# Kernel tuning notes

Measured on AMD Instinct MI355X. Metric: run time of the kernel, lower is better.

Reference implementation:

```python
import jax, jax.numpy as jnp
import numpy as np

N = 100000
D = 100
E = 1600000


def setup_inputs() -> dict:
    key = jax.random.key(0)
    k1, k2, k3, k4 = jax.random.split(key, 4)
    embedding = jax.random.normal(k1, (N, D), dtype=jnp.float32)
    adj_rows = jax.random.randint(k2, (E,), 0, N, dtype=jnp.int32)
    adj_cols = jax.random.randint(k3, (E,), 0, N, dtype=jnp.int32)
    adj_vals = jax.random.uniform(k4, (E,), dtype=jnp.float32)
    return {
        "embedding": embedding,
        "adj_rows": adj_rows,
        "adj_cols": adj_cols,
        "adj_vals": adj_vals,
        "layer_num": 3,
    }


def _spmm(rows, cols, vals, x):
    # sparse [N,N] @ dense [N,D] via gather + weighted segment-sum scatter
    msgs = x[cols] * vals[:, None]           # [E, D]
    return jax.ops.segment_sum(msgs, rows, num_segments=N)  # [N, D]


def reference(embedding, adj_rows, adj_cols, adj_vals, layer_num):
    # out = sum_{i=0}^{layer_num} A^i x  (accumulate hops, including layer 0)
    h = embedding
    acc = embedding
    for _ in range(layer_num):
        h = _spmm(adj_rows, adj_cols, adj_vals, h)
        acc = acc + h
    return acc
```

## Files before the change

kernel.cpp:

```cpp
#include <hip/hip_runtime.h>


#define NODES 100000
#define DIM 100
#define DIM4 25
#define CH 16
#define BSHIFT 8
#define NBUCKETS ((NODES + 255) >> 8)
#define NPAD (NBUCKETS << BSHIFT)

typedef _Float16 half4_t __attribute__((ext_vector_type(4)));
typedef _Float16 half8_t __attribute__((ext_vector_type(8)));

__global__ void cvt_hist_kernel(const float4* __restrict__ emb, half4_t* __restrict__ x0,
                                const int* __restrict__ rows, int* __restrict__ bktCount, int E) {
    __shared__ int h[NBUCKETS];
    for (int i = threadIdx.x; i < NBUCKETS; i += blockDim.x) h[i] = 0;
    __syncthreads();
    int stride = gridDim.x * blockDim.x;
    int gid = blockIdx.x * blockDim.x + threadIdx.x;
    for (int i = gid; i < NODES * 32; i += stride) {
        int r = i >> 5, c = i & 31;
        half4_t hv;
        if (c < 25) {
            float4 f = emb[r * 25 + c];
            hv.x = (_Float16)f.x; hv.y = (_Float16)f.y;
            hv.z = (_Float16)f.z; hv.w = (_Float16)f.w;
        } else {
            hv.x = (_Float16)0.f; hv.y = (_Float16)0.f;
            hv.z = (_Float16)0.f; hv.w = (_Float16)0.f;
        }
        x0[i] = hv;
    }
    for (int e = gid; e < E; e += stride)
        atomicAdd(&h[rows[e] >> BSHIFT], 1);
    __syncthreads();
    for (int i = threadIdx.x; i < NBUCKETS; i += blockDim.x)
        if (h[i]) atomicAdd(&bktCount[i], h[i]);
}

__global__ void pass1_kernel(const int* __restrict__ rows, const int* __restrict__ cols,
                             const float* __restrict__ vals,
                             const int* __restrict__ bktCount, int* __restrict__ gCur,
                             int* __restrict__ bktStart,
                             int2* __restrict__ staging, int E) {
    __shared__ int cnt[NBUCKETS];
    __shared__ int bst[NBUCKETS];
    __shared__ int sc[512];
    int t = threadIdx.x;
    for (int i = t; i < NBUCKETS; i += 512) cnt[i] = 0;
    __syncthreads();
    int chunk = (E + gridDim.x - 1) / gridDim.x;
    int s = blockIdx.x * chunk;
    int e = min(E, s + chunk);
    for (int i = s + t; i < e; i += 512)
        atomicAdd(&cnt[rows[i] >> BSHIFT], 1);
    int v = (t < NBUCKETS) ? bktCount[t] : 0;
    sc[t] = v;
    __syncthreads();
    for (int off = 1; off < 512; off <<= 1) {
        int x = (t >= off) ? sc[t - off] : 0;
        __syncthreads();
        sc[t] += x;
        __syncthreads();
    }
    int excl = sc[t] - v;
    if (blockIdx.x == 0) {
        if (t < NBUCKETS) bktStart[t] = excl;
        if (t == 0) bktStart[NBUCKETS] = E;
    }
    if (t < NBUCKETS) {
        int c = cnt[t];
        bst[t] = excl + (c ? atomicAdd(&gCur[t], c) : 0);
        cnt[t] = 0;
    }
    __syncthreads();
    for (int i = s + t; i < e; i += 512) {
        int r = rows[i];
        int b = r >> BSHIFT;
        int pos = bst[b] + atomicAdd(&cnt[b], 1);
        staging[pos] = make_int2(cols[i] | ((r & 255) << 17), __float_as_int(vals[i]));
    }
}

__global__ void pass2_kernel(const int* __restrict__ bktStart, const int2* __restrict__ staging,
                             int* __restrict__ rowstart, int2* __restrict__ csr) {
    __shared__ int hist[256];
    __shared__ int cur[256];
    int b = blockIdx.x, t = threadIdx.x;
    int s = bktStart[b], e = bktStart[b + 1];
    if (t < 256) hist[t] = 0;
    __syncthreads();
    for (int i = s + t; i < e; i += 512)
        atomicAdd(&hist[(staging[i].x >> 17) & 255], 1);
    __syncthreads();
    int v = (t < 256) ? hist[t] : 0;
    if (t < 256) cur[t] = v;
    __syncthreads();
    for (int off = 1; off < 256; off <<= 1) {
        int x = (t >= off && t < 256) ? cur[t - off] : 0;
        __syncthreads();
        if (t < 256) cur[t] += x;
        __syncthreads();
    }
    if (t < 256) {
        int excl = cur[t] - v;
        rowstart[(b << BSHIFT) + t] = s + excl;
        hist[t] = excl;
    }
    __syncthreads();
    for (int i = s + t; i < e; i += 512) {
        int2 rec = staging[i];
        int lr = (rec.x >> 17) & 255;
        int p = atomicAdd(&hist[lr], 1);
        csr[s + p] = make_int2(rec.x & 0x1FFFF, rec.y);
    }
}

__global__ void gather_mid4_kernel(const int* __restrict__ rowstart,
                                   const int2* __restrict__ csr,
                                   const half8_t* __restrict__ x,
                                   half8_t* __restrict__ h) {
    int gid = blockIdx.x * blockDim.x + threadIdx.x;
    int row = gid >> 4, lane = gid & 15;
    if (row >= NODES) return;
    int s = rowstart[row], e = rowstart[row + 1];
    float acc[8] = {0.f, 0.f, 0.f, 0.f, 0.f, 0.f, 0.f, 0.f};
    int i = s;
    for (; i + 3 < e; i += 4) {
        int2 r0 = csr[i], r1 = csr[i + 1], r2 = csr[i + 2], r3 = csr[i + 3];
        half8_t a0 = x[((size_t)r0.x << 4) + lane];
        half8_t a1 = x[((size_t)r1.x << 4) + lane];
        half8_t a2 = x[((size_t)r2.x << 4) + lane];
        half8_t a3 = x[((size_t)r3.x << 4) + lane];
        float v0 = __int_as_float(r0.y), v1 = __int_as_float(r1.y);
        float v2 = __int_as_float(r2.y), v3 = __int_as_float(r3.y);
        #pragma unroll
        for (int k = 0; k < 8; ++k)
            acc[k] += v0 * (float)a0[k] + v1 * (float)a1[k]
                    + v2 * (float)a2[k] + v3 * (float)a3[k];
    }
    for (; i < e; ++i) {
        int2 r0 = csr[i];
        half8_t a0 = x[((size_t)r0.x << 4) + lane];
        float v0 = __int_as_float(r0.y);
        #pragma unroll
        for (int k = 0; k < 8; ++k) acc[k] += v0 * (float)a0[k];
    }
    half8_t hv;
    #pragma unroll
    for (int k = 0; k < 8; ++k) hv[k] = (_Float16)acc[k];
    h[((size_t)row << 4) + lane] = hv;
}

__global__ void gather_mid8_kernel(const int* __restrict__ rowstart,
                                   const int2* __restrict__ csr,
                                   const half8_t* __restrict__ x,
                                   half8_t* __restrict__ h) {
    int gid = blockIdx.x * blockDim.x + threadIdx.x;
    int row = gid >> 4, lane = gid & 15;
    if (row >= NODES) return;
    int s = rowstart[row], e = rowstart[row + 1];
    float acc[8] = {0.f, 0.f, 0.f, 0.f, 0.f, 0.f, 0.f, 0.f};
    int i = s;
    for (; i + 7 < e; i += 8) {
        int2 rr[8];
        #pragma unroll
        for (int j = 0; j < 8; ++j) rr[j] = csr[i + j];
        half8_t aa[8];
        #pragma unroll
        for (int j = 0; j < 8; ++j) aa[j] = x[((size_t)rr[j].x << 4) + lane];
        #pragma unroll
        for (int j = 0; j < 8; ++j) {
            float v = __int_as_float(rr[j].y);
            #pragma unroll
            for (int k = 0; k < 8; ++k) acc[k] += v * (float)aa[j][k];
        }
    }
    for (; i < e; ++i) {
        int2 r0 = csr[i];
        half8_t a0 = x[((size_t)r0.x << 4) + lane];
        float v0 = __int_as_float(r0.y);
        #pragma unroll
        for (int k = 0; k < 8; ++k) acc[k] += v0 * (float)a0[k];
    }
    half8_t hv;
    #pragma unroll
    for (int k = 0; k < 8; ++k) hv[k] = (_Float16)acc[k];
    h[((size_t)row << 4) + lane] = hv;
}

__global__ void gather_last_kernel(const int* __restrict__ rowstart,
                                   const int2* __restrict__ csr,
                                   const half8_t* __restrict__ x,
                                   const half8_t* __restrict__ x0,
                                   const half8_t* __restrict__ h1,
                                   const half8_t* __restrict__ h2,
                                   float4* __restrict__ out) {
    int gid = blockIdx.x * blockDim.x + threadIdx.x;
    int row = gid >> 4, lane = gid & 15;
    if (row >= NODES) return;
    int s = rowstart[row], e = rowstart[row + 1];
    float acc[8] = {0.f, 0.f, 0.f, 0.f, 0.f, 0.f, 0.f, 0.f};
    int i = s;
    for (; i + 7 < e; i += 8) {
        int2 rr[8];
        #pragma unroll
        for (int j = 0; j < 8; ++j) rr[j] = csr[i + j];
        half8_t aa[8];
        #pragma unroll
        for (int j = 0; j < 8; ++j) aa[j] = x[((size_t)rr[j].x << 4) + lane];
        #pragma unroll
        for (int j = 0; j < 8; ++j) {
            float v = __int_as_float(rr[j].y);
            #pragma unroll
            for (int k = 0; k < 8; ++k) acc[k] += v * (float)aa[j][k];
        }
    }
    for (; i < e; ++i) {
        int2 r0 = csr[i];
        half8_t a0 = x[((size_t)r0.x << 4) + lane];
        float v0 = __int_as_float(r0.y);
        #pragma unroll
        for (int k = 0; k < 8; ++k) acc[k] += v0 * (float)a0[k];
    }
    size_t pidx = ((size_t)row << 4) + lane;
    half8_t xe = x0[pidx], a1 = h1[pidx], a2 = h2[pidx];
    int f4 = row * DIM4 + lane * 2;
    if (lane < 13) {
        float4 o0;
        o0.x = acc[0] + (float)xe[0] + (float)a1[0] + (float)a2[0];
        o0.y = acc[1] + (float)xe[1] + (float)a1[1] + (float)a2[1];
        o0.z = acc[2] + (float)xe[2] + (float)a1[2] + (float)a2[2];
        o0.w = acc[3] + (float)xe[3] + (float)a1[3] + (float)a2[3];
        out[f4] = o0;
    }
    if (lane < 12) {
        float4 o1;
        o1.x = acc[4] + (float)xe[4] + (float)a1[4] + (float)a2[4];
        o1.y = acc[5] + (float)xe[5] + (float)a1[5] + (float)a2[5];
        o1.z = acc[6] + (float)xe[6] + (float)a1[6] + (float)a2[6];
        o1.w = acc[7] + (float)xe[7] + (float)a1[7] + (float)a2[7];
        out[f4 + 1] = o1;
    }
}

extern "C" void kernel_launch(void* const* d_in, const int* in_sizes, int n_in,
                              void* d_out, int out_size, void* d_ws, size_t ws_size,
                              hipStream_t stream) {
    const float* emb  = (const float*)d_in[0];
    const int*   rows = (const int*)  d_in[1];
    const int*   cols = (const int*)  d_in[2];
    const float* vals = (const float*)d_in[3];
    const int E = in_sizes[1];

    const size_t ndp_bytes = (size_t)NODES * 128 * sizeof(_Float16);

    char* w = (char*)d_ws;
    half8_t* x0p      = (half8_t*)w;  w += ndp_bytes;
    half8_t* h1p      = (half8_t*)w;  w += ndp_bytes;
    half8_t* h2p      = (half8_t*)w;  w += ndp_bytes;
    int2*    staging  = (int2*)h2p;
    int2*    csr      = (int2*)   w;  w += (size_t)E * sizeof(int2);
    int*     rowstart = (int*)    w;  w += (size_t)(NPAD + 256) * sizeof(int);
    int*     bktCount = (int*)    w;  w += 512 * sizeof(int);
    int*     gCur     = (int*)    w;  w += 512 * sizeof(int);
    int*     bktStart = (int*)    w;  w += 512 * sizeof(int);

    float4* out = (float4*)d_out;

    hipMemsetAsync(bktCount, 0, 1024 * sizeof(int), stream);
    cvt_hist_kernel<<<1024, 256, 0, stream>>>((const float4*)emb, (half4_t*)x0p,
                                              rows, bktCount, E);
    pass1_kernel<<<256, 512, 0, stream>>>(rows, cols, vals, bktCount, gCur, bktStart,
                                          staging, E);
    pass2_kernel<<<NBUCKETS, 512, 0, stream>>>(bktStart, staging, rowstart, csr);

    const long long threads = (long long)NODES * 16;
    dim3 gGrid((unsigned)((threads + 255) / 256)), gBlock(256);
    gather_mid4_kernel<<<gGrid, gBlock, 0, stream>>>(rowstart, csr, x0p, h1p);
    gather_mid8_kernel<<<gGrid, gBlock, 0, stream>>>(rowstart, csr, h1p, h2p);
    gather_last_kernel<<<gGrid, gBlock, 0, stream>>>(rowstart, csr, h2p, x0p, h1p, h2p, out);
}
```

Before: 363.4 us.

## Stage pass1 bucket scatter in shared memory for coalesced staging writes

Pass1 now handles fixed 3200-edge chunks across 500 blocks instead of 256 large chunks. Each block first sorts its edges by bucket in shared memory using a local prefix scan, then writes them out as contiguous runs per bucket. The aim is to replace scattered 8-byte global writes with mostly contiguous ones and to raise parallelism. The cost is an extra block scan, more shared memory per block (about 40KB, which may limit occupancy) and more atomics on gCur, one per block.

```diff
diff --git a/kernel.cpp b/kernel.cpp
--- a/kernel.cpp
+++ b/kernel.cpp
@@ -8,6 +8,7 @@
 #define BSHIFT 8
 #define NBUCKETS ((NODES + 255) >> 8)
 #define NPAD (NBUCKETS << BSHIFT)
+#define P1CHUNK 3200
 
 typedef _Float16 half4_t __attribute__((ext_vector_type(4)));
 typedef _Float16 half8_t __attribute__((ext_vector_type(8)));
@@ -44,15 +45,18 @@
                              const int* __restrict__ bktCount, int* __restrict__ gCur,
                              int* __restrict__ bktStart,
                              int2* __restrict__ staging, int E) {
+    __shared__ int2 srt[P1CHUNK];
+    __shared__ unsigned short bb2[P1CHUNK];
     __shared__ int cnt[NBUCKETS];
+    __shared__ int base[NBUCKETS];
+    __shared__ int lcur[NBUCKETS];
     __shared__ int bst[NBUCKETS];
     __shared__ int sc[512];
     int t = threadIdx.x;
     for (int i = t; i < NBUCKETS; i += 512) cnt[i] = 0;
     __syncthreads();
-    int chunk = (E + gridDim.x - 1) / gridDim.x;
-    int s = blockIdx.x * chunk;
-    int e = min(E, s + chunk);
+    int s = blockIdx.x * P1CHUNK;
+    int e = min(E, s + P1CHUNK);
     for (int i = s + t; i < e; i += 512)
         atomicAdd(&cnt[rows[i] >> BSHIFT], 1);
     int v = (t < NBUCKETS) ? bktCount[t] : 0;
@@ -72,14 +76,34 @@
     if (t < NBUCKETS) {
         int c = cnt[t];
         bst[t] = excl + (c ? atomicAdd(&gCur[t], c) : 0);
-        cnt[t] = 0;
+    }
+    __syncthreads();
+    int lv = (t < NBUCKETS) ? cnt[t] : 0;
+    sc[t] = lv;
+    __syncthreads();
+    for (int off = 1; off < 512; off <<= 1) {
+        int x = (t >= off) ? sc[t - off] : 0;
+        __syncthreads();
+        sc[t] += x;
+        __syncthreads();
+    }
+    if (t < NBUCKETS) {
+        base[t] = sc[t] - lv;
+        lcur[t] = sc[t] - lv;
     }
     __syncthreads();
     for (int i = s + t; i < e; i += 512) {
         int r = rows[i];
         int b = r >> BSHIFT;
-        int pos = bst[b] + atomicAdd(&cnt[b], 1);
-        staging[pos] = make_int2(cols[i] | ((r & 255) << 17), __float_as_int(vals[i]));
+        int pos = atomicAdd(&lcur[b], 1);
+        srt[pos] = make_int2(cols[i] | ((r & 255) << 17), __float_as_int(vals[i]));
+        bb2[pos] = (unsigned short)b;
+    }
+    __syncthreads();
+    int n = e - s;
+    for (int i = t; i < n; i += 512) {
+        int b = bb2[i];
+        staging[bst[b] + (i - base[b])] = srt[i];
     }
 }
 
@@ -272,8 +296,9 @@
     hipMemsetAsync(bktCount, 0, 1024 * sizeof(int), stream);
     cvt_hist_kernel<<<1024, 256, 0, stream>>>((const float4*)emb, (half4_t*)x0p,
                                               rows, bktCount, E);
-    pass1_kernel<<<256, 512, 0, stream>>>(rows, cols, vals, bktCount, gCur, bktStart,
-                                          staging, E);
+    int p1grid = (E + P1CHUNK - 1) / P1CHUNK;
+    pass1_kernel<<<p1grid, 512, 0, stream>>>(rows, cols, vals, bktCount, gCur, bktStart,
+                                             staging, E);
     pass2_kernel<<<NBUCKETS, 512, 0, stream>>>(bktStart, staging, rowstart, csr);
 
     const long long threads = (long long)NODES * 16;
```

New measurement: 361.6 us. About the same (-0.5%).
